# Kernel tuning notes

Measured on AMD Instinct MI355X. Metric: run time of the kernel, lower is better.

The kernel has to match this reference:

```python
import jax, jax.numpy as jnp
import numpy as np

HIDDEN = 64
MLP_HID = 40

def setup_inputs() -> dict:
    key = jax.random.key(0)
    ks = jax.random.split(key, 9)
    B, T, H = 256, 4096, HIDDEN
    s_ih = 1.0 / np.sqrt(H)
    inputs = jax.random.normal(ks[0], (B, T), dtype=jnp.float32)
    W_ih = jax.random.uniform(ks[1], (4 * H, 1), jnp.float32, -s_ih, s_ih)
    W_hh = jax.random.uniform(ks[2], (4 * H, H), jnp.float32, -s_ih, s_ih)
    b_ih = jax.random.uniform(ks[3], (4 * H,), jnp.float32, -s_ih, s_ih)
    b_hh = jax.random.uniform(ks[4], (4 * H,), jnp.float32, -s_ih, s_ih)
    s1 = 1.0 / np.sqrt(H + 1)
    W1 = jax.random.uniform(ks[5], (MLP_HID, H + 1), jnp.float32, -s1, s1)
    b1 = jax.random.uniform(ks[6], (MLP_HID,), jnp.float32, -s1, s1)
    s2 = 1.0 / np.sqrt(MLP_HID)
    W2 = jax.random.uniform(ks[7], (1, MLP_HID), jnp.float32, -s2, s2)
    b2 = jax.random.uniform(ks[8], (1,), jnp.float32, -s2, s2)
    return {"inputs": inputs, "W_ih": W_ih, "W_hh": W_hh, "b_ih": b_ih,
            "b_hh": b_hh, "W1": W1, "b1": b1, "W2": W2, "b2": b2}

def _lstm(inputs, W_ih, W_hh, b_ih, b_hh):
    # inputs: [B, T]; input_size = 1 so x projection is an outer product.
    B, T = inputs.shape
    H = W_hh.shape[1]
    # x_proj: [T, B, 4H] (time-major for scan)
    x_proj = inputs.T[:, :, None] * W_ih[:, 0][None, None, :] + (b_ih + b_hh)

    def step(carry, xp):
        h, c = carry
        gates = xp + h @ W_hh.T  # [B, 4H]
        i, f, g, o = jnp.split(gates, 4, axis=-1)
        i = jax.nn.sigmoid(i)
        f = jax.nn.sigmoid(f)
        g = jnp.tanh(g)
        o = jax.nn.sigmoid(o)
        c = f * c + i * g
        h = o * jnp.tanh(c)
        return (h, c), h

    h0 = jnp.zeros((B, H), inputs.dtype)
    c0 = jnp.zeros((B, H), inputs.dtype)
    (_, _), hs = jax.lax.scan(step, (h0, c0), x_proj)
    return hs.transpose(1, 0, 2)  # [B, T, H]

def reference(inputs, W_ih, W_hh, b_ih, b_hh, W1, b1, W2, b2):
    hiddens = _lstm(inputs, W_ih, W_hh, b_ih, b_hh)          # [B, T, H]
    combined = jnp.concatenate([hiddens, inputs[:, :, None]], axis=2)  # [B, T, H+1]
    z = jax.nn.sigmoid(combined @ W1.T + b1)                  # [B, T, 40]
    y = z @ W2.T + b2                                         # [B, T, 1]
    return y[:, :, 0]
```

## Files before the change

kernel.cpp:

```cpp
#include <hip/hip_runtime.h>

#define HIDDEN  64
#define T_LEN   4096
#define CHUNK   32
#define MLP_HID 40
#define HP      68
#define W1P     68
#define ZP      41

typedef float v2f __attribute__((ext_vector_type(2)));
typedef float v4f __attribute__((ext_vector_type(4)));

#define LO2(x) __builtin_shufflevector(x, x, 0, 1)
#define HI2(x) __builtin_shufflevector(x, x, 2, 3)

__device__ __forceinline__ v2f pk_fma(v2f a, v2f b, v2f c) {
    v2f d;
    asm("v_pk_fma_f32 %0, %1, %2, %3" : "=v"(d) : "v"(a), "v"(b), "v"(c));
    return d;
}
__device__ __forceinline__ float dpp_x1(float v) {
    return __int_as_float(__builtin_amdgcn_update_dpp(
        0, __float_as_int(v), 0xB1, 0xF, 0xF, true));
}
__device__ __forceinline__ float dpp_x2(float v) {
    return __int_as_float(__builtin_amdgcn_update_dpp(
        0, __float_as_int(v), 0x4E, 0xF, 0xF, true));
}
__device__ __forceinline__ float fast_sigmoid(float x) {
    float e = __builtin_amdgcn_exp2f(x * -1.4426950408889634f);
    return __builtin_amdgcn_rcpf(1.0f + e);
}

__global__ __launch_bounds__(256, 1)
void lstm_mlp_kernel(const float* __restrict__ inputs,
                     const float* __restrict__ W_ih,
                     const float* __restrict__ W_hh,
                     const float* __restrict__ b_ih,
                     const float* __restrict__ b_hh,
                     const float* __restrict__ W1,
                     const float* __restrict__ b1,
                     const float* __restrict__ W2,
                     const float* __restrict__ b2,
                     float* __restrict__ out)
{
    __shared__ __align__(16) float x_lds[T_LEN];
    __shared__ __align__(16) float h_hist[CHUNK * HP];
    __shared__ __align__(16) float w1_lds[MLP_HID * W1P];
    __shared__ float b1_lds[MLP_HID];
    __shared__ float w2_lds[MLP_HID];
    __shared__ float z_lds[CHUNK * ZP];

    const int tid = threadIdx.x;
    const int b   = blockIdx.x;
    const int w   = tid >> 6;
    const int l   = tid & 63;
    const int r   = l >> 2;
    const int q   = l & 3;
    const int u   = 16 * w + r;
    const bool q1 = (q & 1) != 0;
    const bool q2 = (q & 2) != 0;
    const bool wlane = (q == 1);

    const float4* in4 = (const float4*)(inputs + (size_t)b * T_LEN);
    float4* x4 = (float4*)x_lds;
    #pragma unroll
    for (int rr = 0; rr < 4; ++rr) x4[tid + 256 * rr] = in4[tid + 256 * rr];

    v2f wq2[4][8];
    #pragma unroll
    for (int j = 0; j < 4; ++j) {
        const float4* p = (const float4*)(W_hh + (j * 64 + u) * HIDDEN + 16 * q);
        #pragma unroll
        for (int m = 0; m < 4; ++m) {
            float4 t = p[m];
            wq2[j][2 * m]     = (v2f){t.x, t.y};
            wq2[j][2 * m + 1] = (v2f){t.z, t.w};
        }
    }
    const int   gown = q * 64 + u;
    const float wq   = W_ih[gown];
    const float bq   = b_ih[gown] + b_hh[gown];
    const float m_c  = (q == 2) ?  2.8853900817779268f : -1.4426950408889634f;
    const float a_c  = (q == 2) ? -2.0f : 1.0f;
    const float d_c  = (q == 2) ?  1.0f : 0.0f;
    const float b2v  = b2[0];

    for (int p = tid; p < MLP_HID * 65; p += 256) {
        int row = p / 65, col = p - row * 65;
        w1_lds[row * W1P + col] = W1[p];
    }
    if (tid < MLP_HID) { b1_lds[tid] = b1[tid]; w2_lds[tid] = W2[tid]; }
    if (tid < HIDDEN)  h_hist[31 * HP + tid] = 0.0f;
    float c = 0.0f;
    __syncthreads();

    float* outb = out + (size_t)b * T_LEN;
    const float* hq_base = h_hist + 16 * q;
    float*       hwp     = h_hist + u;

    for (int tc = 0; tc < T_LEN / CHUNK; ++tc) {
        const float* xcb = x_lds + tc * CHUNK;

        #pragma unroll
        for (int tt = 0; tt < CHUNK; ++tt) {
            const int rp = (tt + CHUNK - 1) & (CHUNK - 1);
            const v4f* h4 = (const v4f*)(hq_base + rp * HP);
            v4f ha = h4[0], hb = h4[1], hc = h4[2], hd = h4[3];
            float xv = xcb[tt];

            float acc[4];
            #pragma unroll
            for (int j = 0; j < 4; ++j) {
                v2f p0 = LO2(ha) * wq2[j][0];
                v2f p1 = HI2(ha) * wq2[j][1];
                p0 = pk_fma(LO2(hb), wq2[j][2], p0);
                p1 = pk_fma(HI2(hb), wq2[j][3], p1);
                p0 = pk_fma(LO2(hc), wq2[j][4], p0);
                p1 = pk_fma(HI2(hc), wq2[j][5], p1);
                p0 = pk_fma(LO2(hd), wq2[j][6], p0);
                p1 = pk_fma(HI2(hd), wq2[j][7], p1);
                v2f s = p0 + p1;
                acc[j] = s.x + s.y;
            }
            #pragma unroll
            for (int j = 0; j < 4; ++j) acc[j] += dpp_x1(acc[j]);
            float t0 = q1 ? acc[1] : acc[0];
            float t1 = q1 ? acc[3] : acc[2];
            float s_own  = q2 ? t1 : t0;
            float s_part = q2 ? t0 : t1;
            float tot = s_own + dpp_x2(s_part);

            float pre = tot + fmaf(xv, wq, bq);
            float act = fmaf(a_c, __builtin_amdgcn_rcpf(
                              1.0f + __builtin_amdgcn_exp2f(m_c * pre)), d_c);

            float recv = dpp_x2(act);
            float p    = act * recv;
            float e0 = q2 ? recv : act;
            float e  = q1 ? e0 : p;
            float rr = dpp_x1(e);
            float fv = q1 ? e : rr;
            float ig = q1 ? rr : e;
            c = fmaf(fv, c, ig);
            float th = fmaf(-2.0f, __builtin_amdgcn_rcpf(
                             1.0f + __builtin_amdgcn_exp2f(2.8853900817779268f * c)), 1.0f);
            float ov = q2 ? act : recv;
            float hn = ov * th;
            if (wlane) hwp[tt * HP] = hn;
            __syncthreads();
        }

        {
            int tbase = tc * CHUNK;
            int tl = tid >> 3, j0 = tid & 7;
            float4 hh[16];
            const float4* hr = (const float4*)(h_hist + tl * HP);
            #pragma unroll
            for (int m = 0; m < 16; ++m) hh[m] = hr[m];
            float xc = x_lds[tbase + tl];
            #pragma unroll
            for (int jj = 0; jj < 5; ++jj) {
                int j = j0 + 8 * jj;
                const float4* w1r = (const float4*)(w1_lds + j * W1P);
                float a0 = b1_lds[j], a1 = 0.f, a2 = 0.f, a3 = 0.f;
                #pragma unroll
                for (int m = 0; m < 16; ++m) {
                    float4 wv = w1r[m];
                    a0 = fmaf(hh[m].x, wv.x, a0);
                    a1 = fmaf(hh[m].y, wv.y, a1);
                    a2 = fmaf(hh[m].z, wv.z, a2);
                    a3 = fmaf(hh[m].w, wv.w, a3);
                }
                float zacc = ((a0 + a1) + (a2 + a3)) + xc * w1_lds[j * W1P + 64];
                z_lds[tl * ZP + j] = fast_sigmoid(zacc);
            }
            __syncthreads();
            if (tid < CHUNK) {
                float y = b2v;
                #pragma unroll
                for (int j = 0; j < MLP_HID; ++j)
                    y = fmaf(w2_lds[j], z_lds[tid * ZP + j], y);
                outb[tbase + tid] = y;
            }
        }
    }
}

extern "C" void kernel_launch(void* const* d_in, const int* in_sizes, int n_in,
                              void* d_out, int out_size, void* d_ws, size_t ws_size,
                              hipStream_t stream) {
    const float* inputs = (const float*)d_in[0];
    const float* W_ih   = (const float*)d_in[1];
    const float* W_hh   = (const float*)d_in[2];
    const float* b_ih   = (const float*)d_in[3];
    const float* b_hh   = (const float*)d_in[4];
    const float* W1     = (const float*)d_in[5];
    const float* b1     = (const float*)d_in[6];
    const float* W2     = (const float*)d_in[7];
    const float* b2     = (const float*)d_in[8];
    float* out = (float*)d_out;

    lstm_mlp_kernel<<<dim3(256), dim3(256), 0, stream>>>(
        inputs, W_ih, W_hh, b_ih, b_hh, W1, b1, W2, b2, out);
}
```

Baseline: 1.428 ms.

## Switch recurrent and MLP matvecs to fp16 dot2 with fp16 hidden history

Stores W_hh, W1 and the hidden-state history as packed fp16 pairs and replaces the packed fp32 FMAs with v_dot2_f32_f16 instructions that accumulate in fp32. This halves the LDS bytes read per timestep for h and the register footprint of the recurrent weights, and cuts the per-gate instruction count on the serial critical path. The MLP matvec uses the same fp16 layout. The cost is reduced precision in the recurrent state over 4096 steps, which may affect accuracy.

```diff
diff --git a/kernel.cpp b/kernel.cpp
--- a/kernel.cpp
+++ b/kernel.cpp
@@ -1,23 +1,25 @@
 #include <hip/hip_runtime.h>
 
-#define HIDDEN  64
-#define T_LEN   4096
-#define CHUNK   32
+#define T_LEN  4096
+#define CHUNK  32
 #define MLP_HID 40
-#define HP      68
-#define W1P     68
-#define ZP      41
-
-typedef float v2f __attribute__((ext_vector_type(2)));
-typedef float v4f __attribute__((ext_vector_type(4)));
-
-#define LO2(x) __builtin_shufflevector(x, x, 0, 1)
-#define HI2(x) __builtin_shufflevector(x, x, 2, 3)
-
-__device__ __forceinline__ v2f pk_fma(v2f a, v2f b, v2f c) {
-    v2f d;
-    asm("v_pk_fma_f32 %0, %1, %2, %3" : "=v"(d) : "v"(a), "v"(b), "v"(c));
-    return d;
+#define HROW16 80
+#define HRU4   10
+#define W1H2P  40
+#define W1U4   10
+#define ZP     41
+
+typedef float  v4f __attribute__((ext_vector_type(4)));
+typedef _Float16 h2 __attribute__((ext_vector_type(2)));
+
+__device__ __forceinline__ float fdot2(h2 a, h2 b, float c) {
+    return __builtin_amdgcn_fdot2(a, b, c, false);
+}
+__device__ __forceinline__ h2 pack16(float a, float b) {
+    return (h2){(_Float16)a, (_Float16)b};
+}
+__device__ __forceinline__ h2 bch2(unsigned int x) {
+    return __builtin_bit_cast(h2, x);
 }
 __device__ __forceinline__ float dpp_x1(float v) {
     return __int_as_float(__builtin_amdgcn_update_dpp(
@@ -44,9 +46,10 @@
                      const float* __restrict__ b2,
                      float* __restrict__ out)
 {
-    __shared__ __align__(16) float x_lds[T_LEN];
-    __shared__ __align__(16) float h_hist[CHUNK * HP];
-    __shared__ __align__(16) float w1_lds[MLP_HID * W1P];
+    __shared__ __align__(16) float    x_lds[T_LEN];
+    __shared__ __align__(16) _Float16 h16_lds[CHUNK * HROW16];
+    __shared__ __align__(16) h2       w1h_lds[MLP_HID * W1H2P];
+    __shared__ float w1x_lds[MLP_HID];
     __shared__ float b1_lds[MLP_HID];
     __shared__ float w2_lds[MLP_HID];
     __shared__ float z_lds[CHUNK * ZP];
@@ -65,17 +68,17 @@
     const float4* in4 = (const float4*)(inputs + (size_t)b * T_LEN);
     float4* x4 = (float4*)x_lds;
     #pragma unroll
-    for (int rr = 0; rr < 4; ++rr) x4[tid + 256 * rr] = in4[tid + 256 * rr];
-
-    v2f wq2[4][8];
+    for (int rr2 = 0; rr2 < 4; ++rr2) x4[tid + 256 * rr2] = in4[tid + 256 * rr2];
+
+    h2 wd[4][8];
     #pragma unroll
     for (int j = 0; j < 4; ++j) {
-        const float4* p = (const float4*)(W_hh + (j * 64 + u) * HIDDEN + 16 * q);
+        const v4f* p = (const v4f*)(W_hh + (j * 64 + u) * 64 + 16 * q);
         #pragma unroll
         for (int m = 0; m < 4; ++m) {
-            float4 t = p[m];
-            wq2[j][2 * m]     = (v2f){t.x, t.y};
-            wq2[j][2 * m + 1] = (v2f){t.z, t.w};
+            v4f t = p[m];
+            wd[j][2 * m]     = pack16(t.x, t.y);
+            wd[j][2 * m + 1] = pack16(t.z, t.w);
         }
     }
     const int   gown = q * 64 + u;
@@ -86,18 +89,21 @@
     const float d_c  = (q == 2) ?  1.0f : 0.0f;
     const float b2v  = b2[0];
 
-    for (int p = tid; p < MLP_HID * 65; p += 256) {
-        int row = p / 65, col = p - row * 65;
-        w1_lds[row * W1P + col] = W1[p];
-    }
-    if (tid < MLP_HID) { b1_lds[tid] = b1[tid]; w2_lds[tid] = W2[tid]; }
-    if (tid < HIDDEN)  h_hist[31 * HP + tid] = 0.0f;
+    for (int p = tid; p < MLP_HID * 32; p += 256) {
+        int j = p >> 5, kk = p & 31;
+        w1h_lds[j * W1H2P + kk] = pack16(W1[j * 65 + 2 * kk], W1[j * 65 + 2 * kk + 1]);
+    }
+    if (tid < MLP_HID) {
+        w1x_lds[tid] = W1[tid * 65 + 64];
+        b1_lds[tid]  = b1[tid];
+        w2_lds[tid]  = W2[tid];
+    }
+    if (tid < 64) h16_lds[31 * HROW16 + tid] = (_Float16)0.0f;
     float c = 0.0f;
     __syncthreads();
 
     float* outb = out + (size_t)b * T_LEN;
-    const float* hq_base = h_hist + 16 * q;
-    float*       hwp     = h_hist + u;
+    const uint4* h16u4 = (const uint4*)h16_lds;
 
     for (int tc = 0; tc < T_LEN / CHUNK; ++tc) {
         const float* xcb = x_lds + tc * CHUNK;
@@ -105,23 +111,24 @@
         #pragma unroll
         for (int tt = 0; tt < CHUNK; ++tt) {
             const int rp = (tt + CHUNK - 1) & (CHUNK - 1);
-            const v4f* h4 = (const v4f*)(hq_base + rp * HP);
-            v4f ha = h4[0], hb = h4[1], hc = h4[2], hd = h4[3];
+            const uint4* hr = h16u4 + rp * HRU4 + 2 * q;
+            uint4 hqa = hr[0], hqb = hr[1];
+            h2 p0 = bch2(hqa.x), p1 = bch2(hqa.y), p2 = bch2(hqa.z), p3 = bch2(hqa.w);
+            h2 p4 = bch2(hqb.x), p5 = bch2(hqb.y), p6 = bch2(hqb.z), p7 = bch2(hqb.w);
             float xv = xcb[tt];
 
             float acc[4];
             #pragma unroll
             for (int j = 0; j < 4; ++j) {
-                v2f p0 = LO2(ha) * wq2[j][0];
-                v2f p1 = HI2(ha) * wq2[j][1];
-                p0 = pk_fma(LO2(hb), wq2[j][2], p0);
-                p1 = pk_fma(HI2(hb), wq2[j][3], p1);
-                p0 = pk_fma(LO2(hc), wq2[j][4], p0);
-                p1 = pk_fma(HI2(hc), wq2[j][5], p1);
-                p0 = pk_fma(LO2(hd), wq2[j][6], p0);
-                p1 = pk_fma(HI2(hd), wq2[j][7], p1);
-                v2f s = p0 + p1;
-                acc[j] = s.x + s.y;
+                float aa = fdot2(p0, wd[j][0], 0.0f);
+                float ab = fdot2(p1, wd[j][1], 0.0f);
+                aa = fdot2(p2, wd[j][2], aa);
+                ab = fdot2(p3, wd[j][3], ab);
+                aa = fdot2(p4, wd[j][4], aa);
+                ab = fdot2(p5, wd[j][5], ab);
+                aa = fdot2(p6, wd[j][6], aa);
+                ab = fdot2(p7, wd[j][7], ab);
+                acc[j] = aa + ab;
             }
             #pragma unroll
             for (int j = 0; j < 4; ++j) acc[j] += dpp_x1(acc[j]);
@@ -147,32 +154,33 @@
                              1.0f + __builtin_amdgcn_exp2f(2.8853900817779268f * c)), 1.0f);
             float ov = q2 ? act : recv;
             float hn = ov * th;
-            if (wlane) hwp[tt * HP] = hn;
+            if (wlane) h16_lds[tt * HROW16 + u] = (_Float16)hn;
             __syncthreads();
         }
 
         {
             int tbase = tc * CHUNK;
             int tl = tid >> 3, j0 = tid & 7;
-            float4 hh[16];
-            const float4* hr = (const float4*)(h_hist + tl * HP);
-            #pragma unroll
-            for (int m = 0; m < 16; ++m) hh[m] = hr[m];
+            uint4 hh[8];
+            const uint4* hrow = h16u4 + tl * HRU4;
+            #pragma unroll
+            for (int m = 0; m < 8; ++m) hh[m] = hrow[m];
             float xc = x_lds[tbase + tl];
+            const uint4* w1u4 = (const uint4*)w1h_lds;
             #pragma unroll
             for (int jj = 0; jj < 5; ++jj) {
                 int j = j0 + 8 * jj;
-                const float4* w1r = (const float4*)(w1_lds + j * W1P);
-                float a0 = b1_lds[j], a1 = 0.f, a2 = 0.f, a3 = 0.f;
+                const uint4* wrow = w1u4 + j * W1U4;
+                float za = b1_lds[j], zb = 0.f;
                 #pragma unroll
-                for (int m = 0; m < 16; ++m) {
-                    float4 wv = w1r[m];
-                    a0 = fmaf(hh[m].x, wv.x, a0);
-                    a1 = fmaf(hh[m].y, wv.y, a1);
-                    a2 = fmaf(hh[m].z, wv.z, a2);
-                    a3 = fmaf(hh[m].w, wv.w, a3);
+                for (int m = 0; m < 8; ++m) {
+                    uint4 wv = wrow[m];
+                    za = fdot2(bch2(hh[m].x), bch2(wv.x), za);
+                    zb = fdot2(bch2(hh[m].y), bch2(wv.y), zb);
+                    za = fdot2(bch2(hh[m].z), bch2(wv.z), za);
+                    zb = fdot2(bch2(hh[m].w), bch2(wv.w), zb);
                 }
-                float zacc = ((a0 + a1) + (a2 + a3)) + xc * w1_lds[j * W1P + 64];
+                float zacc = (za + zb) + xc * w1x_lds[j];
                 z_lds[tl * ZP + j] = fast_sigmoid(zacc);
             }
             __syncthreads();
```

After: 1.563 ms. 9.4% more time.
